# Kernel optimization log

Hardware: AMD Instinct MI355X
Metric: run time of the kernel (lower is better)

The kernel has to match this reference:

```python
import jax, jax.numpy as jnp
import numpy as np

N, E, B, F, H = 400000, 1600000, 8192, 64, 96


def gcn_conv(x, src, dst, W, b, n):
    # PyG GCNConv: x' = D^-1/2 (A+I) D^-1/2 (x W) + b
    x = x @ W
    loop = jnp.arange(n)
    s = jnp.concatenate([src, loop])
    d = jnp.concatenate([dst, loop])
    deg = jax.ops.segment_sum(jnp.ones_like(d, x.dtype), d, num_segments=n)
    dinv = jnp.where(deg > 0, jax.lax.rsqrt(deg), 0.0)
    norm = dinv[s] * dinv[d]  # [E+N]
    return jax.ops.segment_sum(norm[:, None] * x[s], d, num_segments=n) + b


def forward_convs(x, src, dst, Ws, bs, n):
    for i in range(len(Ws)):
        x = gcn_conv(x, src, dst, Ws[i], bs[i], n)
        if i < len(Ws) - 1:
            x = jax.nn.relu(x)
    return x


def att_pool(x, batch, W1, b1, W2, b2, nb):
    # GlobalAttention: gate = Lin(F,F)->ReLU->Lin(F,1); segment softmax; weighted sum
    g = (jax.nn.relu(x @ W1 + b1) @ W2 + b2)[:, 0]  # [N]
    gmax = jax.ops.segment_max(g, batch, num_segments=nb)
    e = jnp.exp(g - gmax[batch])
    denom = jax.ops.segment_sum(e, batch, num_segments=nb)
    a = e / denom[batch]
    return jax.ops.segment_sum(a[:, None] * x, batch, num_segments=nb)


def mean_pool(x, batch, nb):
    s = jax.ops.segment_sum(x, batch, num_segments=nb)
    cnt = jax.ops.segment_sum(jnp.ones_like(batch, x.dtype), batch, num_segments=nb)
    return s / jnp.maximum(cnt, 1.0)[:, None]


def setup_inputs() -> dict:
    key = jax.random.key(0)
    ks = jax.random.split(key, 32)
    inp = {
        "x_p": jax.random.normal(ks[0], (N, F), jnp.float32),
        "x_d": jax.random.normal(ks[1], (N, F), jnp.float32),
        "edge_attr_p": jax.random.normal(ks[2], (E, 8), jnp.float32),
        "edge_attr_d": jax.random.normal(ks[3], (E, 8), jnp.float32),
        "edge_index_p": jax.random.randint(ks[4], (2, E), 0, N),
        "edge_index_d": jax.random.randint(ks[5], (2, E), 0, N),
        "x_p_batch": jnp.sort(jax.random.randint(ks[6], (N,), 0, B)),
        "x_d_batch": jnp.sort(jax.random.randint(ks[7], (N,), 0, B)),
    }
    def lin(k, fi, fo):
        bnd = 1.0 / np.sqrt(fi)
        k1, k2 = jax.random.split(k)
        return (jax.random.uniform(k1, (fi, fo), jnp.float32, -bnd, bnd),
                jax.random.uniform(k2, (fo,), jnp.float32, -bnd, bnd))
    inp["gate_W1"], inp["gate_b1"] = lin(ks[8], F, F)
    inp["gate_W2"], inp["gate_b2"] = lin(ks[9], F, 1)
    dims = [(F, H), (H, H), (H, H)]
    for side, base in (("p", 10), ("d", 13)):
        for i, (fi, fo) in enumerate(dims):
            W, b = lin(ks[base + i], fi, fo)
            inp[f"conv{side}_W{i}"], inp[f"conv{side}_b{i}"] = W, b
    inp["lin_W0"], inp["lin_b0"] = lin(ks[16], 2 * H + 2 * F, H)
    inp["lin_W1"], inp["lin_b1"] = lin(ks[17], H, 1)
    return inp


def reference(x_p, x_d, edge_attr_p, edge_attr_d, edge_index_p, edge_index_d,
              x_p_batch, x_d_batch, gate_W1, gate_b1, gate_W2, gate_b2,
              convp_W0, convp_b0, convp_W1, convp_b1, convp_W2, convp_b2,
              convd_W0, convd_b0, convd_W1, convd_b1, convd_W2, convd_b2,
              lin_W0, lin_b0, lin_W1, lin_b1):
    n, nb = x_p.shape[0], B
    xp_att = att_pool(x_p, x_p_batch, gate_W1, gate_b1, gate_W2, gate_b2, nb)
    xd_att = att_pool(x_d, x_d_batch, gate_W1, gate_b1, gate_W2, gate_b2, nb)
    xp = forward_convs(x_p, edge_index_p[0], edge_index_p[1],
                       [convp_W0, convp_W1, convp_W2], [convp_b0, convp_b1, convp_b2], n)
    xd = forward_convs(x_d, edge_index_d[0], edge_index_d[1],
                       [convd_W0, convd_W1, convd_W2], [convd_b0, convd_b1, convd_b2], n)
    xp = mean_pool(xp, x_p_batch, nb)
    xd = mean_pool(xd, x_d_batch, nb)
    x = jnp.concatenate([xp, xd, xp_att, xd_att], axis=1)  # [B, 2H+2F]
    # dropout p=0.5 is identity in eval mode
    x = jax.nn.relu(x @ lin_W0 + lin_b0)
    return x @ lin_W1 + lin_b1  # [B, 1]
```

## Files before the change

### kernel.cpp

```cpp
#include <hip/hip_runtime.h>

#define NN 400000
#define EE 1600000
#define NB 8192

typedef float vf4 __attribute__((ext_vector_type(4)));
typedef float vf2 __attribute__((ext_vector_type(2)));

__global__ void k_seg(const int* __restrict__ batch, int* __restrict__ start){
  int b = blockIdx.x*256 + threadIdx.x;
  if (b > NB) return;
  int lo = 0, hi = NN;
  while (lo < hi){ int mid = (lo+hi)>>1; if (batch[mid] < b) lo = mid+1; else hi = mid; }
  start[b] = lo;
}

__global__ __launch_bounds__(256) void k_gate(const float* __restrict__ x,
    const float* __restrict__ W1, const float* __restrict__ b1,
    const float* __restrict__ W2, const float* __restrict__ b2,
    float* __restrict__ g){
  __shared__ __align__(16) float sX[64*68];
  __shared__ __align__(16) float sW[64*64];
  __shared__ float sB[128];
  __shared__ float sRed[64*17];
  const int tid = threadIdx.x;
  const int r0 = blockIdx.x << 6;
  for (int i = tid; i < 4096; i += 256) sW[i] = W1[i];
  if (tid < 64) sB[tid] = b1[tid];
  else if (tid < 128) sB[tid] = W2[tid-64];
  for (int i = tid; i < 4096; i += 256){
    int r = i >> 6, k = i & 63;
    sX[k*68 + r] = x[(size_t)r0*64 + i];
  }
  __syncthreads();
  const int tx = tid & 15;
  const int ty = tid >> 4;
  float acc[4][4];
  #pragma unroll
  for (int i = 0; i < 4; ++i)
    #pragma unroll
    for (int j = 0; j < 4; ++j) acc[i][j] = 0.f;
  for (int k = 0; k < 64; ++k){
    vf4 a = *(const vf4*)&sX[k*68 + ty*4];
    vf4 w = *(const vf4*)&sW[k*64 + tx*4];
    #pragma unroll
    for (int i = 0; i < 4; ++i)
      #pragma unroll
      for (int j = 0; j < 4; ++j)
        acc[i][j] = fmaf(a[i], w[j], acc[i][j]);
  }
  #pragma unroll
  for (int i = 0; i < 4; ++i){
    float p = 0.f;
    #pragma unroll
    for (int j = 0; j < 4; ++j){
      int c = tx*4 + j;
      p = fmaf(fmaxf(acc[i][j] + sB[c], 0.f), sB[64+c], p);
    }
    sRed[(ty*4+i)*17 + tx] = p;
  }
  __syncthreads();
  if (tid < 64){
    float s = 0.f;
    #pragma unroll
    for (int j = 0; j < 16; ++j) s += sRed[tid*17 + j];
    g[r0 + tid] = s + b2[0];
  }
}

__global__ __launch_bounds__(64) void k_att(const float* __restrict__ x, const float* __restrict__ g,
    const int* __restrict__ start, float* __restrict__ att){
  int b = blockIdx.x, lane = threadIdx.x;
  int s0 = start[b], s1 = start[b+1];
  if (s1 <= s0){ att[b*64+lane] = 0.f; return; }
  float m = -3.0e38f;
  for (int i = s0+lane; i < s1; i += 64) m = fmaxf(m, g[i]);
  #pragma unroll
  for (int off = 32; off; off >>= 1) m = fmaxf(m, __shfl_xor(m, off));
  float s = 0.f;
  for (int i = s0+lane; i < s1; i += 64) s += expf(g[i]-m);
  #pragma unroll
  for (int off = 32; off; off >>= 1) s += __shfl_xor(s, off);
  float acc = 0.f;
  for (int i = s0; i < s1; ++i)
    acc = fmaf(expf(g[i]-m), x[(size_t)i*64+lane], acc);
  att[b*64+lane] = acc / s;
}

__global__ void k_zero(int* __restrict__ degI, int* __restrict__ gc){
  int i = blockIdx.x*256 + threadIdx.x;
  if (i < NN) degI[i] = 0;
  if (i == 0) *gc = 0;
}
__global__ void k_count(const int* __restrict__ dst, int* __restrict__ degI){
  int e = blockIdx.x*256 + threadIdx.x;
  if (e < EE) atomicAdd(&degI[dst[e]], 1);
}
__global__ __launch_bounds__(256) void k_alloc(const int* __restrict__ degI, int* __restrict__ gc,
    int* __restrict__ base, int* __restrict__ cursor, float* __restrict__ dinv){
  int i = blockIdx.x*256 + threadIdx.x;
  int lane = threadIdx.x & 63;
  int d = (i < NN) ? degI[i] : 0;
  int incl = d;
  #pragma unroll
  for (int off = 1; off < 64; off <<= 1){
    int t = __shfl_up(incl, off);
    if (lane >= off) incl += t;
  }
  int waveTotal = __shfl(incl, 63);
  int wbase = 0;
  if (lane == 63) wbase = atomicAdd(gc, waveTotal);
  wbase = __shfl(wbase, 63);
  if (i < NN){
    int b = wbase + incl - d;
    base[i] = b; cursor[i] = b;
    dinv[i] = 1.f / sqrtf((float)d + 1.f);
  }
}
__global__ void k_fillcsr(const int* __restrict__ src, const int* __restrict__ dst,
                          const float* __restrict__ dinv,
                          int* __restrict__ cursor, int2* __restrict__ csr2){
  int e = blockIdx.x*256 + threadIdx.x;
  if (e >= EE) return;
  int s = src[e];
  int p = atomicAdd(&cursor[dst[e]], 1);
  csr2[p] = make_int2(s, __float_as_int(dinv[s]));
}

template<int K, bool RELU>
__global__ __launch_bounds__(256) void k_gemm(const float* __restrict__ in,
    const float* __restrict__ W, const float* __restrict__ bias, float* __restrict__ out){
  __shared__ __align__(16) float sIn[K*68];
  __shared__ __align__(16) float sW[K*96];
  __shared__ float sB[96];
  const int tid = threadIdx.x;
  const int r0 = blockIdx.x << 6;
  for (int i = tid; i < K*96; i += 256) sW[i] = W[i];
  if (tid < 96) sB[tid] = bias[tid];
  for (int i = tid; i < 64*K; i += 256){
    int r = i / K, k = i - r*K;
    sIn[k*68 + r] = in[(size_t)r0*K + i];
  }
  __syncthreads();
  const int tx = tid & 15;
  const int ty = tid >> 4;
  float acc[4][6];
  #pragma unroll
  for (int i = 0; i < 4; ++i)
    #pragma unroll
    for (int j = 0; j < 6; ++j) acc[i][j] = 0.f;
  for (int k = 0; k < K; ++k){
    vf4 a   = *(const vf4*)&sIn[k*68 + ty*4];
    vf2 w01 = *(const vf2*)&sW[k*96 + tx*6];
    vf2 w23 = *(const vf2*)&sW[k*96 + tx*6 + 2];
    vf2 w45 = *(const vf2*)&sW[k*96 + tx*6 + 4];
    float w[6] = {w01[0], w01[1], w23[0], w23[1], w45[0], w45[1]};
    #pragma unroll
    for (int i = 0; i < 4; ++i)
      #pragma unroll
      for (int j = 0; j < 6; ++j)
        acc[i][j] = fmaf(a[i], w[j], acc[i][j]);
  }
  #pragma unroll
  for (int i = 0; i < 4; ++i){
    size_t row = r0 + ty*4 + i;
    #pragma unroll
    for (int j = 0; j < 6; ++j){
      float v = acc[i][j] + sB[tx*6 + j];
      if (RELU) v = fmaxf(v, 0.f);
      out[row*96 + tx*6 + j] = v;
    }
  }
}

__global__ __launch_bounds__(256) void k_gather96(const float* __restrict__ xw,
    const int2* __restrict__ csr2, const int* __restrict__ base, const int* __restrict__ degI,
    const float* __restrict__ dinv, float* __restrict__ out){
  const int grp  = threadIdx.x >> 5;
  const int lane = threadIdx.x & 31;
  const int i = (blockIdx.x << 3) + grp;
  const bool act = lane < 24;
  const vf4* __restrict__ xw4 = (const vf4*)xw;
  const float di = dinv[i];
  const int b0 = base[i], cnt = degI[i];
  vf4 s = {0.f,0.f,0.f,0.f};
  if (act) s = di * xw4[(size_t)i*24 + lane];
  for (int t = 0; t < cnt; t += 8){
    int2 e[8]; float w[8];
    #pragma unroll
    for (int k = 0; k < 8; ++k){
      int p = t + k;
      int q = p < cnt ? p : cnt-1;
      e[k] = csr2[b0 + q];
      w[k] = (p < cnt) ? __int_as_float(e[k].y) : 0.f;
    }
    if (act){
      #pragma unroll
      for (int k = 0; k < 8; ++k){
        vf4 v = xw4[(size_t)e[k].x*24 + lane];
        s += w[k]*v;
      }
    }
  }
  if (act){
    vf4 r = di * s;
    ((vf4*)out)[(size_t)i*24 + lane] = r;
  }
}

__global__ __launch_bounds__(256) void k_gather64(const float* __restrict__ x,
    const int2* __restrict__ csr2, const int* __restrict__ base, const int* __restrict__ degI,
    const float* __restrict__ dinv, float* __restrict__ out){
  const int grp  = threadIdx.x >> 4;
  const int lane = threadIdx.x & 15;
  const int i = (blockIdx.x << 4) + grp;
  const vf4* __restrict__ x4 = (const vf4*)x;
  const float di = dinv[i];
  const int b0 = base[i], cnt = degI[i];
  vf4 s = di * x4[(size_t)i*16 + lane];
  for (int t = 0; t < cnt; t += 8){
    int2 e[8]; float w[8];
    #pragma unroll
    for (int k = 0; k < 8; ++k){
      int p = t + k;
      int q = p < cnt ? p : cnt-1;
      e[k] = csr2[b0 + q];
      w[k] = (p < cnt) ? __int_as_float(e[k].y) : 0.f;
    }
    #pragma unroll
    for (int k = 0; k < 8; ++k){
      vf4 v = x4[(size_t)e[k].x*16 + lane];
      s += w[k]*v;
    }
  }
  vf4 r = di * s;
  ((vf4*)out)[(size_t)i*16 + lane] = r;
}

__global__ __launch_bounds__(128) void k_mean(const float* __restrict__ h,
    const int* __restrict__ start, float* __restrict__ mean){
  int b = blockIdx.x, f = threadIdx.x;
  if (f >= 96) return;
  int s0 = start[b], s1 = start[b+1];
  float acc = 0.f;
  for (int i = s0; i < s1; ++i) acc += h[(size_t)i*96+f];
  mean[b*96+f] = acc / fmaxf((float)(s1-s0), 1.f);
}

__global__ __launch_bounds__(128) void k_final(const float* __restrict__ meanP, const float* __restrict__ meanD,
    const float* __restrict__ attP, const float* __restrict__ attD,
    const float* __restrict__ W0, const float* __restrict__ b0,
    const float* __restrict__ W1, const float* __restrict__ b1,
    float* __restrict__ out){
  __shared__ float cat[320];
  __shared__ float hb[96];
  int b = blockIdx.x, tid = threadIdx.x;
  if (tid < 96){ cat[tid] = meanP[b*96+tid]; cat[96+tid] = meanD[b*96+tid]; }
  if (tid < 64){ cat[192+tid] = attP[b*64+tid]; cat[256+tid] = attD[b*64+tid]; }
  __syncthreads();
  if (tid < 96){
    float acc = b0[tid];
    for (int k = 0; k < 320; ++k) acc = fmaf(cat[k], W0[k*96+tid], acc);
    hb[tid] = fmaxf(acc, 0.f) * W1[tid];
  }
  __syncthreads();
  if (tid == 0){
    float y = b1[0];
    for (int j = 0; j < 96; ++j) y += hb[j];
    out[b] = y;
  }
}

extern "C" void kernel_launch(void* const* d_in, const int* in_sizes, int n_in,
                              void* d_out, int out_size, void* d_ws, size_t ws_size,
                              hipStream_t stream){
  const float* x_p = (const float*)d_in[0];
  const float* x_d = (const float*)d_in[1];
  const int* ei_p = (const int*)d_in[4];
  const int* ei_d = (const int*)d_in[5];
  const int* batch_p = (const int*)d_in[6];
  const int* batch_d = (const int*)d_in[7];
  const float* gW1 = (const float*)d_in[8];
  const float* gb1 = (const float*)d_in[9];
  const float* gW2 = (const float*)d_in[10];
  const float* gb2 = (const float*)d_in[11];
  const float* cW[2][3] = {{(const float*)d_in[12],(const float*)d_in[14],(const float*)d_in[16]},
                           {(const float*)d_in[18],(const float*)d_in[20],(const float*)d_in[22]}};
  const float* cB[2][3] = {{(const float*)d_in[13],(const float*)d_in[15],(const float*)d_in[17]},
                           {(const float*)d_in[19],(const float*)d_in[21],(const float*)d_in[23]}};
  const float* lW0 = (const float*)d_in[24];
  const float* lb0 = (const float*)d_in[25];
  const float* lW1 = (const float*)d_in[26];
  const float* lb1 = (const float*)d_in[27];
  float* out = (float*)d_out;

  float* fws = (float*)d_ws;
  size_t off = 0;
  float* A     = fws + off; off += (size_t)NN*96;
  float* Bf    = fws + off; off += (size_t)NN*96;
  float* dinv  = fws + off; off += NN;
  float* g     = fws + off; off += NN;
  float* attP  = fws + off; off += (size_t)NB*64;
  float* attD  = fws + off; off += (size_t)NB*64;
  float* meanP = fws + off; off += (size_t)NB*96;
  float* meanD = fws + off; off += (size_t)NB*96;
  int2* csr2  = (int2*)(fws + off);
  int* iws = (int*)(csr2 + EE);
  int* segP   = iws;             iws += NB+1;
  int* segD   = iws;             iws += NB+1;
  int* degI   = iws;             iws += NN;
  int* base   = iws;             iws += NN;
  int* cursor = iws;             iws += NN;
  int* gc     = iws;             iws += 1;

  k_seg<<<(NB+1+255)/256, 256, 0, stream>>>(batch_p, segP);
  k_seg<<<(NB+1+255)/256, 256, 0, stream>>>(batch_d, segD);

  for (int side = 0; side < 2; ++side){
    const float* x  = side ? x_d : x_p;
    const int* src = side ? ei_d : ei_p;
    const int* dst = src + EE;
    const int* seg = side ? segD : segP;
    float* att  = side ? attD : attP;
    float* mean = side ? meanD : meanP;

    k_gate<<<NN/64, 256, 0, stream>>>(x, gW1, gb1, gW2, gb2, g);
    k_att<<<NB, 64, 0, stream>>>(x, g, seg, att);

    k_zero   <<<(NN+255)/256, 256, 0, stream>>>(degI, gc);
    k_count  <<<(EE+255)/256, 256, 0, stream>>>(dst, degI);
    k_alloc  <<<(NN+255)/256, 256, 0, stream>>>(degI, gc, base, cursor, dinv);
    k_fillcsr<<<(EE+255)/256, 256, 0, stream>>>(src, dst, dinv, cursor, csr2);

    k_gather64<<<NN/16, 256, 0, stream>>>(x, csr2, base, degI, dinv, A);
    k_gemm<64,true ><<<NN/64, 256, 0, stream>>>(A, cW[side][0], cB[side][0], Bf);
    k_gather96<<<NN/8, 256, 0, stream>>>(Bf, csr2, base, degI, dinv, A);
    k_gemm<96,true ><<<NN/64, 256, 0, stream>>>(A, cW[side][1], cB[side][1], Bf);
    k_gather96<<<NN/8, 256, 0, stream>>>(Bf, csr2, base, degI, dinv, A);
    k_gemm<96,false><<<NN/64, 256, 0, stream>>>(A, cW[side][2], cB[side][2], Bf);

    k_mean<<<NB, 128, 0, stream>>>(Bf, seg, mean);
  }
  k_final<<<NB, 128, 0, stream>>>(meanP, meanD, attP, attD, lW0, lb0, lW1, lb1, out);
}
```

Measured before the change: 2.471 ms.

## Apply final conv weight after mean pooling instead of per node

The last GCN layer's linear transform is moved past the mean pool, since mean(xW+b) = mean(x)W+b. The pooled aggregated features, 8192 rows, are multiplied by W instead of all 400k nodes, removing a full node-level GEMM per side. Empty segments are zeroed to match the original mean pool, which returns 0 for them. It adds a small workspace buffer and changes the floating-point summation order.

Result: faster. 2.285 ms (-7.5%).

```diff
diff --git a/kernel.cpp b/kernel.cpp
--- a/kernel.cpp
+++ b/kernel.cpp
@@ -169,6 +169,53 @@
       float v = acc[i][j] + sB[tx*6 + j];
       if (RELU) v = fmaxf(v, 0.f);
       out[row*96 + tx*6 + j] = v;
+    }
+  }
+}
+
+__global__ __launch_bounds__(256) void k_gemm_pool(const float* __restrict__ in,
+    const float* __restrict__ W, const float* __restrict__ bias,
+    const int* __restrict__ start, float* __restrict__ out){
+  constexpr int K = 96;
+  __shared__ __align__(16) float sIn[K*68];
+  __shared__ __align__(16) float sW[K*96];
+  __shared__ float sB[96];
+  const int tid = threadIdx.x;
+  const int r0 = blockIdx.x << 6;
+  for (int i = tid; i < K*96; i += 256) sW[i] = W[i];
+  if (tid < 96) sB[tid] = bias[tid];
+  for (int i = tid; i < 64*K; i += 256){
+    int r = i / K, k = i - r*K;
+    sIn[k*68 + r] = in[(size_t)r0*K + i];
+  }
+  __syncthreads();
+  const int tx = tid & 15;
+  const int ty = tid >> 4;
+  float acc[4][6];
+  #pragma unroll
+  for (int i = 0; i < 4; ++i)
+    #pragma unroll
+    for (int j = 0; j < 6; ++j) acc[i][j] = 0.f;
+  for (int k = 0; k < K; ++k){
+    vf4 a   = *(const vf4*)&sIn[k*68 + ty*4];
+    vf2 w01 = *(const vf2*)&sW[k*96 + tx*6];
+    vf2 w23 = *(const vf2*)&sW[k*96 + tx*6 + 2];
+    vf2 w45 = *(const vf2*)&sW[k*96 + tx*6 + 4];
+    float w[6] = {w01[0], w01[1], w23[0], w23[1], w45[0], w45[1]};
+    #pragma unroll
+    for (int i = 0; i < 4; ++i)
+      #pragma unroll
+      for (int j = 0; j < 6; ++j)
+        acc[i][j] = fmaf(a[i], w[j], acc[i][j]);
+  }
+  #pragma unroll
+  for (int i = 0; i < 4; ++i){
+    int row = r0 + ty*4 + i;
+    bool nz = start[row+1] > start[row];
+    #pragma unroll
+    for (int j = 0; j < 6; ++j){
+      float v = nz ? (acc[i][j] + sB[tx*6 + j]) : 0.f;
+      out[(size_t)row*96 + tx*6 + j] = v;
     }
   }
 }
@@ -304,6 +351,7 @@
   float* attD  = fws + off; off += (size_t)NB*64;
   float* meanP = fws + off; off += (size_t)NB*96;
   float* meanD = fws + off; off += (size_t)NB*96;
+  float* poolT = fws + off; off += (size_t)NB*96;
   int2* csr2  = (int2*)(fws + off);
   int* iws = (int*)(csr2 + EE);
   int* segP   = iws;             iws += NB+1;
@@ -337,9 +385,8 @@
     k_gather96<<<NN/8, 256, 0, stream>>>(Bf, csr2, base, degI, dinv, A);
     k_gemm<96,true ><<<NN/64, 256, 0, stream>>>(A, cW[side][1], cB[side][1], Bf);
     k_gather96<<<NN/8, 256, 0, stream>>>(Bf, csr2, base, degI, dinv, A);
-    k_gemm<96,false><<<NN/64, 256, 0, stream>>>(A, cW[side][2], cB[side][2], Bf);
-
-    k_mean<<<NB, 128, 0, stream>>>(Bf, seg, mean);
+    k_mean<<<NB, 128, 0, stream>>>(A, seg, poolT);
+    k_gemm_pool<<<NB/64, 256, 0, stream>>>(poolT, cW[side][2], cB[side][2], seg, mean);
   }
   k_final<<<NB, 128, 0, stream>>>(meanP, meanD, attP, attD, lW0, lb0, lW1, lb1, out);
 }
```
